# Performance work log

Measured on AMD Instinct MI355X. Metric: run time of the kernel, lower is better.

The kernel has to match this reference:

```python
import jax, jax.numpy as jnp
import numpy as np

B, C, L = 4, 64, 4096
RED = 4          # reduction -> q/k channels = C // RED = 16
N_HASHES = 4
HASH_BUCKETS = min(L // 4, 32)  # = 32, matches torch code
EPS = 1e-5


def _conv1x1(x, W, b):
    # x: [B, Cin, L], W: [Cout, Cin], b: [Cout]
    return jnp.einsum('bcl,oc->bol', x, W) + b[None, :, None]


def setup_inputs() -> dict:
    key = jax.random.key(0)
    ks = jax.random.split(key, 12)
    Cq = C // RED
    x = jax.random.normal(ks[0], (B, C, L), dtype=jnp.float32)
    hash_idx = jax.random.randint(ks[1], (B, N_HASHES, L), 0, HASH_BUCKETS, dtype=jnp.int32)
    sC = 1.0 / np.sqrt(C)
    Wq = jax.random.normal(ks[2], (Cq, C), dtype=jnp.float32) * sC
    bq = jax.random.normal(ks[3], (Cq,), dtype=jnp.float32) * 0.01
    Wk = jax.random.normal(ks[4], (Cq, C), dtype=jnp.float32) * sC
    bk = jax.random.normal(ks[5], (Cq,), dtype=jnp.float32) * 0.01
    Wv = jax.random.normal(ks[6], (C, C), dtype=jnp.float32) * sC
    bv = jax.random.normal(ks[7], (C,), dtype=jnp.float32) * 0.01
    Wo = jax.random.normal(ks[8], (C, C), dtype=jnp.float32) * sC
    bo = jax.random.normal(ks[9], (C,), dtype=jnp.float32) * 0.01
    gamma = jax.random.normal(ks[10], (1,), dtype=jnp.float32)  # nonzero so attn path matters
    bn_w = jnp.ones((C,), dtype=jnp.float32)
    bn_b = jnp.zeros((C,), dtype=jnp.float32)
    return dict(x=x, hash_idx=hash_idx, Wq=Wq, bq=bq, Wk=Wk, bk=bk,
                Wv=Wv, bv=bv, Wo=Wo, bo=bo, gamma=gamma, bn_w=bn_w, bn_b=bn_b)


def reference(x, hash_idx, Wq, bq, Wk, bk, Wv, bv, Wo, bo, gamma, bn_w, bn_b):
    # 1x1 conv projections
    q = _conv1x1(x, Wq, bq)   # [B, C/RED, L]
    k = _conv1x1(x, Wk, bk)   # [B, C/RED, L]
    v = _conv1x1(x, Wv, bv)   # [B, C, L]

    qT = q.transpose(0, 2, 1)  # [B, L, Cq]
    kT = k.transpose(0, 2, 1)
    vT = v.transpose(0, 2, 1)  # [B, L, C]

    # raw scores are hash-independent; only the bucket mask changes per hash
    scores = jnp.einsum('bic,bjc->bij', qT, kT)  # [B, L, L], no sqrt(d) scaling (matches torch)

    n_hashes = hash_idx.shape[1]
    acc = jnp.zeros_like(vT)
    for h in range(n_hashes):  # small fixed loop
        idx = hash_idx[:, h, :]                       # [B, L]
        mask = idx[:, :, None] == idx[:, None, :]     # same-bucket mask [B, L, L]
        s = jnp.where(mask, scores, -1e9)
        attn = jax.nn.softmax(s, axis=-1)             # within-bucket softmax (diag always valid)
        acc = acc + jnp.einsum('bij,bjc->bic', attn, vT)
    attn_out = (acc / n_hashes).transpose(0, 2, 1)    # [B, C, L], averaged over hashes

    out = _conv1x1(attn_out, Wo, bo)
    out = gamma * out + x                             # residual with learned scalar

    # BatchNorm1d, training mode: biased batch stats over (B, L) per channel
    mean = out.mean(axis=(0, 2), keepdims=True)
    var = out.var(axis=(0, 2), keepdims=True)
    out = (out - mean) * jax.lax.rsqrt(var + EPS)
    out = out * bn_w[None, :, None] + bn_b[None, :, None]
    return out
```

## Files before the change

### kernel.cpp

```cpp
#include <hip/hip_runtime.h>
#include <math.h>

#define Bn 4
#define Cn 64
#define Ln 4096
#define CQ 16
#define NH 4
#define NB 32
#define EPSV 1e-5f

#define MAXS 384
#define CH2 64
#define KSTR 20
#define VSTR 64

#define QSPLIT 2
#define QSTRIDE (64*QSPLIT)

#define QSZ   (Bn*Ln*CQ)
#define VSZ   (Bn*Ln*Cn)
#define ACCSZ (Bn*Ln*Cn)
#define NBH   (Bn*NH)

#define OFF_K   QSZ
#define OFF_V   (2*QSZ)
#define OFF_ACC (2*QSZ + VSZ)

#define LOG2E 1.44269504088896f

__global__ __launch_bounds__(256) void proj_kernel(
        const float* __restrict__ x,
        const float* __restrict__ Wq, const float* __restrict__ bq,
        const float* __restrict__ Wk, const float* __restrict__ bk,
        const float* __restrict__ Wv, const float* __restrict__ bv,
        float* __restrict__ q, float* __restrict__ k, float* __restrict__ v) {
    __shared__ float sWt[Cn*32];
    __shared__ float sb[32];
    int tid = threadIdx.x;
    int third = blockIdx.x % 3;
    int pg    = blockIdx.x / 3;
    int rbase = third * 32;
    for (int idx = tid; idx < Cn*32; idx += 256) {
        int rr = idx & 31, c = idx >> 5;
        int r = rbase + rr;
        float w;
        if (r < 16)      w = Wq[r*Cn + c];
        else if (r < 32) w = Wk[(r-16)*Cn + c];
        else             w = Wv[(r-32)*Cn + c];
        sWt[c*32 + rr] = w;
    }
    if (tid < 32) {
        int r = rbase + tid;
        sb[tid] = (r < 16) ? bq[r] : (r < 32 ? bk[r-16] : bv[r-32]);
    }
    __syncthreads();
    int p = tid & 63, og = tid >> 6;
    int gp = pg * 64 + p;
    int b = gp >> 12, l = gp & (Ln - 1);
    const float* xp = &x[b*Cn*Ln + l];
    int rr0 = og * 8;
    float val[8];
    #pragma unroll
    for (int i = 0; i < 8; i++) val[i] = sb[rr0 + i];
    #pragma unroll
    for (int c0 = 0; c0 < Cn; c0 += 8) {
        float xv[8];
        #pragma unroll
        for (int i = 0; i < 8; i++) xv[i] = xp[(c0 + i)*Ln];
        #pragma unroll
        for (int i = 0; i < 8; i++) {
            const float* wrow = &sWt[(c0 + i)*32 + rr0];
            #pragma unroll
            for (int j = 0; j < 8; j++) val[j] = fmaf(wrow[j], xv[i], val[j]);
        }
    }
    int f = third*8 + og*2;
    float4 t0 = make_float4(val[0], val[1], val[2], val[3]);
    float4 t1 = make_float4(val[4], val[5], val[6], val[7]);
    float4* q4 = (float4*)&q[gp*CQ];
    float4* k4 = (float4*)&k[gp*CQ];
    float4* v4 = (float4*)&v[gp*Cn];
    if (f < 4)      { q4[f]   = t0; q4[f+1] = t1; }
    else if (f < 8) { k4[f-4] = t0; k4[f-3] = t1; }
    else            { v4[f-8] = t0; v4[f-7] = t1; }
}

__device__ __forceinline__ float quad_reduce_sum(float d) {
    d += __int_as_float(__builtin_amdgcn_mov_dpp(__float_as_int(d), 0xB1, 0xF, 0xF, true));
    d += __int_as_float(__builtin_amdgcn_mov_dpp(__float_as_int(d), 0x4E, 0xF, 0xF, true));
    return d;
}

template<int NS, int MODE>
__device__ __forceinline__ void attn_pass(
        int qbase, int S, int b, int h, int tid, int rem,
        const int* list, float* ks, float* vs,
        const float* __restrict__ q, const float* __restrict__ k,
        const float* __restrict__ v, float* __restrict__ acc) {
    int qd = tid >> 2, c4 = tid & 3;
    float4 qr[NS];
    float4 o[NS][4];
    float lsum[NS];
    int qi[NS], iqr[NS];
    #pragma unroll
    for (int s = 0; s < NS; s++) {
        qi[s] = qbase + QSTRIDE*s + qd;
        iqr[s] = 0;
        lsum[s] = 0.f;
        #pragma unroll
        for (int i = 0; i < 4; i++) o[s][i] = make_float4(0.f,0.f,0.f,0.f);
        if (qi[s] < S) {
            iqr[s] = list[qi[s]];
            const float4* qp = (const float4*)&q[((size_t)b*Ln + iqr[s])*CQ];
            float4 t = qp[c4];
            t.x*=LOG2E; t.y*=LOG2E; t.z*=LOG2E; t.w*=LOG2E;
            qr[s] = t;
        } else {
            qr[s] = make_float4(0.f,0.f,0.f,0.f);
        }
    }
    for (int cc = 0; cc < S; cc += CH2) {
        int nk = min(CH2, S - cc);
        __syncthreads();
        {
            int jj = tid >> 2, cf = tid & 3;
            if (jj < nk) {
                const float4* kp = (const float4*)&k[((size_t)b*Ln + list[cc+jj])*CQ];
                *(float4*)&ks[jj*KSTR + cf*4] = kp[cf];
            }
        }
        #pragma unroll
        for (int uu = 0; uu < 4; uu++) {
            int idx = uu*256 + tid;
            int jj = idx >> 4, cf = idx & 15;
            if (jj < nk) {
                const float4* vp = (const float4*)&v[((size_t)b*Ln + list[cc+jj])*Cn];
                *(float4*)&vs[jj*VSTR + cf*4] = vp[cf];
            }
        }
        __syncthreads();
        if (rem > 0) {
            for (int j = 0; j < nk; j++) {
                float4 kq = *(const float4*)&ks[j*KSTR + c4*4];
                const float4* vp4 = (const float4*)&vs[j*VSTR + c4*16];
                float4 v0 = vp4[0], v1 = vp4[1], v2 = vp4[2], v3 = vp4[3];
                #pragma unroll
                for (int s = 0; s < NS; s++) {
                    float d = qr[s].x*kq.x;
                    d = fmaf(qr[s].y, kq.y, d);
                    d = fmaf(qr[s].z, kq.z, d);
                    d = fmaf(qr[s].w, kq.w, d);
                    d = quad_reduce_sum(d);
                    float pw = __builtin_amdgcn_exp2f(d);
                    lsum[s] += pw;
                    o[s][0].x = fmaf(pw, v0.x, o[s][0].x); o[s][0].y = fmaf(pw, v0.y, o[s][0].y);
                    o[s][0].z = fmaf(pw, v0.z, o[s][0].z); o[s][0].w = fmaf(pw, v0.w, o[s][0].w);
                    o[s][1].x = fmaf(pw, v1.x, o[s][1].x); o[s][1].y = fmaf(pw, v1.y, o[s][1].y);
                    o[s][1].z = fmaf(pw, v1.z, o[s][1].z); o[s][1].w = fmaf(pw, v1.w, o[s][1].w);
                    o[s][2].x = fmaf(pw, v2.x, o[s][2].x); o[s][2].y = fmaf(pw, v2.y, o[s][2].y);
                    o[s][2].z = fmaf(pw, v2.z, o[s][2].z); o[s][2].w = fmaf(pw, v2.w, o[s][2].w);
                    o[s][3].x = fmaf(pw, v3.x, o[s][3].x); o[s][3].y = fmaf(pw, v3.y, o[s][3].y);
                    o[s][3].z = fmaf(pw, v3.z, o[s][3].z); o[s][3].w = fmaf(pw, v3.w, o[s][3].w);
                }
            }
        }
    }
    #pragma unroll
    for (int s = 0; s < NS; s++) {
        if (qi[s] < S) {
            float inv = 1.f / lsum[s];
            #pragma unroll
            for (int i = 0; i < 4; i++) {
                o[s][i].x*=inv; o[s][i].y*=inv; o[s][i].z*=inv; o[s][i].w*=inv;
            }
            if (MODE == 1) {
                float4* ap = (float4*)&acc[((size_t)h*Bn*Ln + b*Ln + iqr[s])*Cn + c4*16];
                ap[0]=o[s][0]; ap[1]=o[s][1]; ap[2]=o[s][2]; ap[3]=o[s][3];
            } else {
                float* ap = &acc[((size_t)b*Ln + iqr[s])*Cn + c4*16];
                #pragma unroll
                for (int i = 0; i < 4; i++) {
                    atomicAdd(&ap[4*i+0], (&o[s][i].x)[0]);
                    atomicAdd(&ap[4*i+1], (&o[s][i].x)[1]);
                    atomicAdd(&ap[4*i+2], (&o[s][i].x)[2]);
                    atomicAdd(&ap[4*i+3], (&o[s][i].x)[3]);
                }
            }
        }
    }
}

template<int MODE>
__global__ __launch_bounds__(256, 4) void attn_kernel(
        const float* __restrict__ q, const float* __restrict__ k,
        const float* __restrict__ v, const int* __restrict__ hidx,
        float* __restrict__ acc) {
    __shared__ int list[MAXS];
    __shared__ float ks[CH2*KSTR];
    __shared__ float vs[CH2*VSTR];
    __shared__ int wtot[4];
    int blk = blockIdx.x;
    int qs = blk >> 9;
    int u  = blk & (NB-1);
    int bh = (blk >> 5) & (NBH-1);
    int b  = bh >> 2;
    int h  = bh & 3;
    int tid = threadIdx.x;

    const int4* hp4 = (const int4*)(&hidx[bh*Ln] + tid*16);
    int hv[16];
    #pragma unroll
    for (int t = 0; t < 4; t++) {
        int4 tmp = hp4[t];
        hv[t*4+0]=tmp.x; hv[t*4+1]=tmp.y; hv[t*4+2]=tmp.z; hv[t*4+3]=tmp.w;
    }
    int myCnt = 0;
    #pragma unroll
    for (int t = 0; t < 16; t++) myCnt += (hv[t] == u);
    int lane = tid & 63, wv = tid >> 6;
    int pre = myCnt;
    #pragma unroll
    for (int d = 1; d < 64; d <<= 1) {
        int t = __shfl_up(pre, d, 64);
        if (lane >= d) pre += t;
    }
    if (lane == 63) wtot[wv] = pre;
    __syncthreads();
    int base = 0;
    #pragma unroll
    for (int w = 0; w < 4; w++) base += (w < wv) ? wtot[w] : 0;
    int Sall = wtot[0] + wtot[1] + wtot[2] + wtot[3];
    int S = min(Sall, MAXS);
    int excl = base + pre - myCnt;
    #pragma unroll
    for (int t = 0; t < 16; t++) {
        if (hv[t] == u) {
            if (excl < MAXS) list[excl] = tid*16 + t;
            excl++;
        }
    }
    __syncthreads();

    int wq0 = (tid >> 6) << 4;
    for (int qbase = qs*64; qbase < S; qbase += 3*QSTRIDE) {
        int rem = S - qbase - wq0;
        if (rem > 2*QSTRIDE)      attn_pass<3,MODE>(qbase,S,b,h,tid,rem,list,ks,vs,q,k,v,acc);
        else if (rem > QSTRIDE)   attn_pass<2,MODE>(qbase,S,b,h,tid,rem,list,ks,vs,q,k,v,acc);
        else                      attn_pass<1,MODE>(qbase,S,b,h,tid,rem,list,ks,vs,q,k,v,acc);
    }
}

template<int MODE>
__global__ __launch_bounds__(256) void outconv_kernel(
        const float* __restrict__ acc, const float* __restrict__ Wo,
        const float* __restrict__ bo, const float* __restrict__ gamma,
        const float* __restrict__ x, float* __restrict__ y) {
    __shared__ float sWt[Cn*Cn];
    __shared__ float sA[Cn*33];
    __shared__ float sb[Cn];
    int tid = threadIdx.x;
    int pg = blockIdx.x;
    for (int idx = tid; idx < Cn*Cn; idx += 256) {
        int o = idx & 63, c = idx >> 6;
        sWt[c*Cn + o] = Wo[o*Cn + c];
    }
    if (tid < Cn) sb[tid] = bo[tid];
    const float4* a4 = (const float4*)&acc[(size_t)pg*32*Cn];
    #pragma unroll
    for (int r = 0; r < 2; r++) {
        int idx = r*256 + tid;
        int p = idx >> 4, c0 = (idx & 15) * 4;
        float4 t = a4[idx];
        if (MODE == 1) {
            float4 t1 = a4[(size_t)ACCSZ/4   + idx];
            float4 t2 = a4[(size_t)ACCSZ/4*2 + idx];
            float4 t3 = a4[(size_t)ACCSZ/4*3 + idx];
            t.x += t1.x + t2.x + t3.x; t.y += t1.y + t2.y + t3.y;
            t.z += t1.z + t2.z + t3.z; t.w += t1.w + t2.w + t3.w;
        }
        sA[(c0+0)*33 + p] = t.x*0.25f;
        sA[(c0+1)*33 + p] = t.y*0.25f;
        sA[(c0+2)*33 + p] = t.z*0.25f;
        sA[(c0+3)*33 + p] = t.w*0.25f;
    }
    __syncthreads();
    float g = gamma[0];
    int p = tid & 31, og = tid >> 5;
    int gp = pg * 32 + p;
    int b = gp >> 12, l = gp & (Ln - 1);
    int o0 = og * 8;
    float val[8];
    #pragma unroll
    for (int i = 0; i < 8; i++) val[i] = sb[o0 + i];
    #pragma unroll
    for (int c = 0; c < Cn; c++) {
        float av = sA[c*33 + p];
        const float* wrow = &sWt[c*Cn + o0];
        #pragma unroll
        for (int i = 0; i < 8; i++) val[i] = fmaf(wrow[i], av, val[i]);
    }
    #pragma unroll
    for (int i = 0; i < 8; i++) {
        int o = o0 + i;
        float yv = fmaf(g, val[i], x[(b*Cn + o)*Ln + l]);
        y[(b*Cn + o)*Ln + l] = yv;
    }
}

__global__ __launch_bounds__(256) void stats_kernel(
        const float* __restrict__ y, float* __restrict__ ssumP, float* __restrict__ ssqP) {
    int c = blockIdx.x >> 2;
    int part = blockIdx.x & 3;
    int tid = threadIdx.x;
    const float4* yp = (const float4*)&y[(part*Cn + c)*Ln];
    float s = 0.f, s2 = 0.f;
    #pragma unroll
    for (int i = 0; i < 4; i++) {
        float4 t = yp[i*256 + tid];
        s  += t.x + t.y + t.z + t.w;
        s2 += t.x*t.x + t.y*t.y + t.z*t.z + t.w*t.w;
    }
    #pragma unroll
    for (int w = 1; w < 64; w <<= 1) {
        s  += __shfl_xor(s,  w, 64);
        s2 += __shfl_xor(s2, w, 64);
    }
    __shared__ float rs[4], rs2[4];
    int wv = tid >> 6;
    if ((tid & 63) == 0) { rs[wv] = s; rs2[wv] = s2; }
    __syncthreads();
    if (tid == 0) {
        ssumP[blockIdx.x] = rs[0]+rs[1]+rs[2]+rs[3];
        ssqP[blockIdx.x]  = rs2[0]+rs2[1]+rs2[2]+rs2[3];
    }
}

__global__ __launch_bounds__(256) void norm_kernel(
        const float* __restrict__ y,
        const float* __restrict__ ssumP, const float* __restrict__ ssqP,
        const float* __restrict__ bnw, const float* __restrict__ bnb,
        float* __restrict__ out) {
    int idx = blockIdx.x * 256 + threadIdx.x;
    int flat = idx * 4;
    int c = (flat / Ln) & 63;
    float s = 0.f, s2 = 0.f;
    #pragma unroll
    for (int hh = 0; hh < 4; hh++) { s += ssumP[c*4+hh]; s2 += ssqP[c*4+hh]; }
    const float n = (float)(Bn*Ln);
    float mu = s / n;
    float var = s2 / n - mu*mu;
    float is = rsqrtf(var + EPSV);
    float w = is * bnw[c];
    float bb = bnb[c] - mu * w;
    float4 t = ((const float4*)y)[idx];
    float4 r;
    r.x = t.x*w + bb; r.y = t.y*w + bb; r.z = t.z*w + bb; r.w = t.w*w + bb;
    ((float4*)out)[idx] = r;
}

extern "C" void kernel_launch(void* const* d_in, const int* in_sizes, int n_in,
                              void* d_out, int out_size, void* d_ws, size_t ws_size,
                              hipStream_t stream) {
    const float* x    = (const float*)d_in[0];
    const int*   hidx = (const int*)  d_in[1];
    const float* Wq   = (const float*)d_in[2];
    const float* bq   = (const float*)d_in[3];
    const float* Wk   = (const float*)d_in[4];
    const float* bk   = (const float*)d_in[5];
    const float* Wv   = (const float*)d_in[6];
    const float* bv   = (const float*)d_in[7];
    const float* Wo   = (const float*)d_in[8];
    const float* bo   = (const float*)d_in[9];
    const float* gam  = (const float*)d_in[10];
    const float* bnw  = (const float*)d_in[11];
    const float* bnb  = (const float*)d_in[12];
    float* out = (float*)d_out;

    float* ws  = (float*)d_ws;
    float* q   = ws;
    float* k   = ws + OFF_K;
    float* v   = ws + OFF_V;
    float* acc = ws + OFF_ACC;
    float* y   = ws;

    const size_t bigNeed = ((size_t)OFF_ACC + 4*(size_t)ACCSZ + 512) * sizeof(float);
    bool big = ws_size >= bigNeed;
    float* ssumP = acc + (big ? 4*(size_t)ACCSZ : (size_t)ACCSZ);
    float* ssqP  = ssumP + 256;

    proj_kernel<<<Bn*Ln/64*3, 256, 0, stream>>>(x, Wq, bq, Wk, bk, Wv, bv, q, k, v);
    if (big) {
        attn_kernel<1><<<NBH*NB*QSPLIT, 256, 0, stream>>>(q, k, v, hidx, acc);
        outconv_kernel<1><<<Bn*Ln/32, 256, 0, stream>>>(acc, Wo, bo, gam, x, y);
    } else {
        hipMemsetAsync(acc, 0, (size_t)ACCSZ*sizeof(float), stream);
        attn_kernel<0><<<NBH*NB*QSPLIT, 256, 0, stream>>>(q, k, v, hidx, acc);
        outconv_kernel<0><<<Bn*Ln/32, 256, 0, stream>>>(acc, Wo, bo, gam, x, y);
    }
    stats_kernel<<<Cn*4, 256, 0, stream>>>(y, ssumP, ssqP);
    norm_kernel<<<Bn*Cn*Ln/4/256, 256, 0, stream>>>(y, ssumP, ssqP, bnw, bnb, out);
}
```

Baseline: 155.2 us.

## Restructure bucket attention to stage whole bucket KV once and split keys across lanes

The attention kernel now launches one block per (batch, hash, bucket) instead of two query-split blocks. It stages the whole bucket's K and V into shared memory in one pass when the bucket fits in 192 entries, and falls back to chunked staging otherwise. Inside a wave, lanes are split across four queries and four key sub-streams; partial sums are combined with DPP row reductions at the end, and only one lane group writes results. This is meant to cut repeated KV staging and per-chunk barriers, at the cost of half as many blocks, a lower occupancy hint, extra reduction shuffles and masked tail handling. Separately, the weight rows in the projection and output-conv kernels are now read from shared memory as float4 loads.

```diff
diff --git a/kernel.cpp b/kernel.cpp
--- a/kernel.cpp
+++ b/kernel.cpp
@@ -10,12 +10,7 @@
 #define EPSV 1e-5f
 
 #define MAXS 384
-#define CH2 64
-#define KSTR 20
-#define VSTR 64
-
-#define QSPLIT 2
-#define QSTRIDE (64*QSPLIT)
+#define SFULL 192
 
 #define QSZ   (Bn*Ln*CQ)
 #define VSZ   (Bn*Ln*Cn)
@@ -69,9 +64,13 @@
         for (int i = 0; i < 8; i++) xv[i] = xp[(c0 + i)*Ln];
         #pragma unroll
         for (int i = 0; i < 8; i++) {
-            const float* wrow = &sWt[(c0 + i)*32 + rr0];
-            #pragma unroll
-            for (int j = 0; j < 8; j++) val[j] = fmaf(wrow[j], xv[i], val[j]);
+            const float4 wa = *(const float4*)&sWt[(c0 + i)*32 + rr0];
+            const float4 wb = *(const float4*)&sWt[(c0 + i)*32 + rr0 + 4];
+            float xvi = xv[i];
+            val[0] = fmaf(wa.x, xvi, val[0]); val[1] = fmaf(wa.y, xvi, val[1]);
+            val[2] = fmaf(wa.z, xvi, val[2]); val[3] = fmaf(wa.w, xvi, val[3]);
+            val[4] = fmaf(wb.x, xvi, val[4]); val[5] = fmaf(wb.y, xvi, val[5]);
+            val[6] = fmaf(wb.z, xvi, val[6]); val[7] = fmaf(wb.w, xvi, val[7]);
         }
     }
     int f = third*8 + og*2;
@@ -91,118 +90,145 @@
     return d;
 }
 
-template<int NS, int MODE>
-__device__ __forceinline__ void attn_pass(
-        int qbase, int S, int b, int h, int tid, int rem,
-        const int* list, float* ks, float* vs,
-        const float* __restrict__ q, const float* __restrict__ k,
-        const float* __restrict__ v, float* __restrict__ acc) {
-    int qd = tid >> 2, c4 = tid & 3;
-    float4 qr[NS];
-    float4 o[NS][4];
-    float lsum[NS];
-    int qi[NS], iqr[NS];
-    #pragma unroll
-    for (int s = 0; s < NS; s++) {
-        qi[s] = qbase + QSTRIDE*s + qd;
-        iqr[s] = 0;
-        lsum[s] = 0.f;
+__device__ __forceinline__ float rowsum16(float x) {
+    x += __int_as_float(__builtin_amdgcn_mov_dpp(__float_as_int(x), 0x114, 0xF, 0xF, true));
+    x += __int_as_float(__builtin_amdgcn_mov_dpp(__float_as_int(x), 0x118, 0xF, 0xF, true));
+    return x;
+}
+
+struct SweepState {
+    float4 qr[4];
+    float4 o[4][4];
+    float  lsum[4];
+    int    ir[4];
+    int    qact[4];
+};
+
+__device__ __forceinline__ void sweep_init(SweepState& st, int q0, int S, int act,
+        const int* list, const float4* Q4, int qq, int c4) {
+    #pragma unroll
+    for (int s = 0; s < 4; s++) {
+        int qi = q0 + s*4 + qq;
+        int a = act && (qi < S);
+        st.qact[s] = a;
+        int r = a ? list[qi] : 0;
+        st.ir[s] = r;
+        float4 t = make_float4(0.f, 0.f, 0.f, 0.f);
+        if (a) {
+            t = Q4[(size_t)r*4 + c4];
+            t.x *= LOG2E; t.y *= LOG2E; t.z *= LOG2E; t.w *= LOG2E;
+        }
+        st.qr[s] = t;
+        st.lsum[s] = 0.f;
         #pragma unroll
-        for (int i = 0; i < 4; i++) o[s][i] = make_float4(0.f,0.f,0.f,0.f);
-        if (qi[s] < S) {
-            iqr[s] = list[qi[s]];
-            const float4* qp = (const float4*)&q[((size_t)b*Ln + iqr[s])*CQ];
-            float4 t = qp[c4];
-            t.x*=LOG2E; t.y*=LOG2E; t.z*=LOG2E; t.w*=LOG2E;
-            qr[s] = t;
-        } else {
-            qr[s] = make_float4(0.f,0.f,0.f,0.f);
-        }
-    }
-    for (int cc = 0; cc < S; cc += CH2) {
-        int nk = min(CH2, S - cc);
-        __syncthreads();
-        {
-            int jj = tid >> 2, cf = tid & 3;
-            if (jj < nk) {
-                const float4* kp = (const float4*)&k[((size_t)b*Ln + list[cc+jj])*CQ];
-                *(float4*)&ks[jj*KSTR + cf*4] = kp[cf];
-            }
-        }
+        for (int tt = 0; tt < 4; tt++) st.o[s][tt] = make_float4(0.f, 0.f, 0.f, 0.f);
+    }
+}
+
+template<bool MASKED>
+__device__ __forceinline__ void kb_step(SweepState& st, int kb, int nkv,
+        const float4* ks4, const float4* vs4, int l15, int kk,
+        int i0, int i1, int i2, int i3) {
+    const float4 kq = ks4[kb*16 + l15];
+    const float4 va = vs4[kb*64 + i0*16 + l15];
+    const float4 vb = vs4[kb*64 + i1*16 + l15];
+    const float4 vc = vs4[kb*64 + i2*16 + l15];
+    const float4 vd = vs4[kb*64 + i3*16 + l15];
+    #pragma unroll
+    for (int s = 0; s < 4; s++) {
+        float d = st.qr[s].x * kq.x;
+        d = fmaf(st.qr[s].y, kq.y, d);
+        d = fmaf(st.qr[s].z, kq.z, d);
+        d = fmaf(st.qr[s].w, kq.w, d);
+        d = quad_reduce_sum(d);
+        float pw = __builtin_amdgcn_exp2f(d);
+        if (MASKED) pw = ((kb*4 + kk) < nkv) ? pw : 0.f;
+        st.lsum[s] += pw;
+        st.o[s][0].x = fmaf(pw, va.x, st.o[s][0].x); st.o[s][0].y = fmaf(pw, va.y, st.o[s][0].y);
+        st.o[s][0].z = fmaf(pw, va.z, st.o[s][0].z); st.o[s][0].w = fmaf(pw, va.w, st.o[s][0].w);
+        st.o[s][1].x = fmaf(pw, vb.x, st.o[s][1].x); st.o[s][1].y = fmaf(pw, vb.y, st.o[s][1].y);
+        st.o[s][1].z = fmaf(pw, vb.z, st.o[s][1].z); st.o[s][1].w = fmaf(pw, vb.w, st.o[s][1].w);
+        st.o[s][2].x = fmaf(pw, vc.x, st.o[s][2].x); st.o[s][2].y = fmaf(pw, vc.y, st.o[s][2].y);
+        st.o[s][2].z = fmaf(pw, vc.z, st.o[s][2].z); st.o[s][2].w = fmaf(pw, vc.w, st.o[s][2].w);
+        st.o[s][3].x = fmaf(pw, vd.x, st.o[s][3].x); st.o[s][3].y = fmaf(pw, vd.y, st.o[s][3].y);
+        st.o[s][3].z = fmaf(pw, vd.z, st.o[s][3].z); st.o[s][3].w = fmaf(pw, vd.w, st.o[s][3].w);
+    }
+}
+
+__device__ __forceinline__ void sweep_keys(SweepState& st, int nk,
+        const float4* ks4, const float4* vs4, int l15, int kk,
+        int i0, int i1, int i2, int i3) {
+    int nf = nk >> 2;
+    for (int kb = 0; kb < nf; kb++)
+        kb_step<false>(st, kb, nk, ks4, vs4, l15, kk, i0, i1, i2, i3);
+    if (nk & 3)
+        kb_step<true>(st, nf, nk, ks4, vs4, l15, kk, i0, i1, i2, i3);
+}
+
+template<int MODE>
+__device__ __forceinline__ void sweep_fin(SweepState& st, float* __restrict__ acc,
+        int b, int h, int qq, int lane, int c4) {
+    #pragma unroll
+    for (int s = 0; s < 4; s++) {
+        st.lsum[s] = rowsum16(st.lsum[s]);
         #pragma unroll
-        for (int uu = 0; uu < 4; uu++) {
-            int idx = uu*256 + tid;
-            int jj = idx >> 4, cf = idx & 15;
-            if (jj < nk) {
-                const float4* vp = (const float4*)&v[((size_t)b*Ln + list[cc+jj])*Cn];
-                *(float4*)&vs[jj*VSTR + cf*4] = vp[cf];
-            }
-        }
-        __syncthreads();
-        if (rem > 0) {
-            for (int j = 0; j < nk; j++) {
-                float4 kq = *(const float4*)&ks[j*KSTR + c4*4];
-                const float4* vp4 = (const float4*)&vs[j*VSTR + c4*16];
-                float4 v0 = vp4[0], v1 = vp4[1], v2 = vp4[2], v3 = vp4[3];
-                #pragma unroll
-                for (int s = 0; s < NS; s++) {
-                    float d = qr[s].x*kq.x;
-                    d = fmaf(qr[s].y, kq.y, d);
-                    d = fmaf(qr[s].z, kq.z, d);
-                    d = fmaf(qr[s].w, kq.w, d);
-                    d = quad_reduce_sum(d);
-                    float pw = __builtin_amdgcn_exp2f(d);
-                    lsum[s] += pw;
-                    o[s][0].x = fmaf(pw, v0.x, o[s][0].x); o[s][0].y = fmaf(pw, v0.y, o[s][0].y);
-                    o[s][0].z = fmaf(pw, v0.z, o[s][0].z); o[s][0].w = fmaf(pw, v0.w, o[s][0].w);
-                    o[s][1].x = fmaf(pw, v1.x, o[s][1].x); o[s][1].y = fmaf(pw, v1.y, o[s][1].y);
-                    o[s][1].z = fmaf(pw, v1.z, o[s][1].z); o[s][1].w = fmaf(pw, v1.w, o[s][1].w);
-                    o[s][2].x = fmaf(pw, v2.x, o[s][2].x); o[s][2].y = fmaf(pw, v2.y, o[s][2].y);
-                    o[s][2].z = fmaf(pw, v2.z, o[s][2].z); o[s][2].w = fmaf(pw, v2.w, o[s][2].w);
-                    o[s][3].x = fmaf(pw, v3.x, o[s][3].x); o[s][3].y = fmaf(pw, v3.y, o[s][3].y);
-                    o[s][3].z = fmaf(pw, v3.z, o[s][3].z); o[s][3].w = fmaf(pw, v3.w, o[s][3].w);
+        for (int t = 0; t < 4; t++) {
+            st.o[s][t].x = rowsum16(st.o[s][t].x);
+            st.o[s][t].y = rowsum16(st.o[s][t].y);
+            st.o[s][t].z = rowsum16(st.o[s][t].z);
+            st.o[s][t].w = rowsum16(st.o[s][t].w);
+        }
+    }
+    if ((lane & 15) < 12) return;
+    #pragma unroll
+    for (int s = 0; s < 4; s++) {
+        if (st.qact[s]) {
+            float inv = 1.f / st.lsum[s];
+            #pragma unroll
+            for (int t = 0; t < 4; t++) {
+                float4 r;
+                r.x = st.o[s][t].x * inv; r.y = st.o[s][t].y * inv;
+                r.z = st.o[s][t].z * inv; r.w = st.o[s][t].w * inv;
+                int ch = ((qq + t) & 3)*16 + c4*4;
+                if (MODE == 1) {
+                    *(float4*)&acc[(((size_t)h*Bn + b)*Ln + st.ir[s])*Cn + ch] = r;
+                } else {
+                    float* ap = &acc[((size_t)b*Ln + st.ir[s])*Cn + ch];
+                    atomicAdd(&ap[0], r.x); atomicAdd(&ap[1], r.y);
+                    atomicAdd(&ap[2], r.z); atomicAdd(&ap[3], r.w);
                 }
             }
         }
     }
-    #pragma unroll
-    for (int s = 0; s < NS; s++) {
-        if (qi[s] < S) {
-            float inv = 1.f / lsum[s];
-            #pragma unroll
-            for (int i = 0; i < 4; i++) {
-                o[s][i].x*=inv; o[s][i].y*=inv; o[s][i].z*=inv; o[s][i].w*=inv;
-            }
-            if (MODE == 1) {
-                float4* ap = (float4*)&acc[((size_t)h*Bn*Ln + b*Ln + iqr[s])*Cn + c4*16];
-                ap[0]=o[s][0]; ap[1]=o[s][1]; ap[2]=o[s][2]; ap[3]=o[s][3];
-            } else {
-                float* ap = &acc[((size_t)b*Ln + iqr[s])*Cn + c4*16];
-                #pragma unroll
-                for (int i = 0; i < 4; i++) {
-                    atomicAdd(&ap[4*i+0], (&o[s][i].x)[0]);
-                    atomicAdd(&ap[4*i+1], (&o[s][i].x)[1]);
-                    atomicAdd(&ap[4*i+2], (&o[s][i].x)[2]);
-                    atomicAdd(&ap[4*i+3], (&o[s][i].x)[3]);
-                }
-            }
-        }
+}
+
+__device__ __forceinline__ void stage_kv(int tid, int nk, int k0, const int* list,
+        const float4* K4, const float4* V4, float4* ks4, float4* vs4) {
+    const float4 z = make_float4(0.f, 0.f, 0.f, 0.f);
+    int nb4 = (nk + 3) >> 2;
+    for (int G = tid; G < nb4*16; G += 256) {
+        int j = G >> 2;
+        ks4[G] = (j < nk) ? K4[(size_t)list[k0 + j]*4 + (G & 3)] : z;
+    }
+    for (int F = tid; F < nb4*64; F += 256) {
+        int kb = F >> 6, ii = (F >> 4) & 3, k2 = (F >> 2) & 3, cc = F & 3;
+        int j = kb*4 + k2;
+        vs4[F] = (j < nk) ? V4[(size_t)list[k0 + j]*16 + ii*4 + cc] : z;
     }
 }
 
 template<int MODE>
-__global__ __launch_bounds__(256, 4) void attn_kernel(
+__global__ __launch_bounds__(256, 2) void attn_kernel(
         const float* __restrict__ q, const float* __restrict__ k,
         const float* __restrict__ v, const int* __restrict__ hidx,
         float* __restrict__ acc) {
     __shared__ int list[MAXS];
-    __shared__ float ks[CH2*KSTR];
-    __shared__ float vs[CH2*VSTR];
     __shared__ int wtot[4];
+    __shared__ float4 ks4[SFULL*4];
+    __shared__ float4 vs4[SFULL*16];
     int blk = blockIdx.x;
-    int qs = blk >> 9;
     int u  = blk & (NB-1);
-    int bh = (blk >> 5) & (NBH-1);
+    int bh = blk >> 5;
     int b  = bh >> 2;
     int h  = bh & 3;
     int tid = threadIdx.x;
@@ -241,12 +267,39 @@
     }
     __syncthreads();
 
-    int wq0 = (tid >> 6) << 4;
-    for (int qbase = qs*64; qbase < S; qbase += 3*QSTRIDE) {
-        int rem = S - qbase - wq0;
-        if (rem > 2*QSTRIDE)      attn_pass<3,MODE>(qbase,S,b,h,tid,rem,list,ks,vs,q,k,v,acc);
-        else if (rem > QSTRIDE)   attn_pass<2,MODE>(qbase,S,b,h,tid,rem,list,ks,vs,q,k,v,acc);
-        else                      attn_pass<1,MODE>(qbase,S,b,h,tid,rem,list,ks,vs,q,k,v,acc);
+    int qq = (lane >> 4) & 3;
+    int kk = (lane >> 2) & 3;
+    int c4 = lane & 3;
+    int l15 = lane & 15;
+    int i0 = qq, i1 = (qq+1)&3, i2 = (qq+2)&3, i3 = (qq+3)&3;
+    const float4* Q4 = (const float4*)&q[(size_t)b*Ln*CQ];
+    const float4* K4 = (const float4*)&k[(size_t)b*Ln*CQ];
+    const float4* V4 = (const float4*)&v[(size_t)b*Ln*Cn];
+
+    if (S <= SFULL) {
+        stage_kv(tid, S, 0, list, K4, V4, ks4, vs4);
+        __syncthreads();
+        for (int q0 = wv*16; q0 < S; q0 += 64) {
+            SweepState st;
+            sweep_init(st, q0, S, 1, list, Q4, qq, c4);
+            sweep_keys(st, S, ks4, vs4, l15, kk, i0, i1, i2, i3);
+            sweep_fin<MODE>(st, acc, b, h, qq, lane, c4);
+        }
+    } else {
+        for (int q0s = 0; q0s < S; q0s += 64) {
+            int q0 = q0s + wv*16;
+            int act = q0 < S;
+            SweepState st;
+            sweep_init(st, q0, S, act, list, Q4, qq, c4);
+            for (int k0 = 0; k0 < S; k0 += SFULL) {
+                int nk = min(SFULL, S - k0);
+                __syncthreads();
+                stage_kv(tid, nk, k0, list, K4, V4, ks4, vs4);
+                __syncthreads();
+                if (act) sweep_keys(st, nk, ks4, vs4, l15, kk, i0, i1, i2, i3);
+            }
+            if (act) sweep_fin<MODE>(st, acc, b, h, qq, lane, c4);
+        }
     }
 }
 
@@ -295,9 +348,12 @@
     #pragma unroll
     for (int c = 0; c < Cn; c++) {
         float av = sA[c*33 + p];
-        const float* wrow = &sWt[c*Cn + o0];
-        #pragma unroll
-        for (int i = 0; i < 8; i++) val[i] = fmaf(wrow[i], av, val[i]);
+        const float4 wa = *(const float4*)&sWt[c*Cn + o0];
+        const float4 wb = *(const float4*)&sWt[c*Cn + o0 + 4];
+        val[0] = fmaf(wa.x, av, val[0]); val[1] = fmaf(wa.y, av, val[1]);
+        val[2] = fmaf(wa.z, av, val[2]); val[3] = fmaf(wa.w, av, val[3]);
+        val[4] = fmaf(wb.x, av, val[4]); val[5] = fmaf(wb.y, av, val[5]);
+        val[6] = fmaf(wb.z, av, val[6]); val[7] = fmaf(wb.w, av, val[7]);
     }
     #pragma unroll
     for (int i = 0; i < 8; i++) {
@@ -390,11 +446,11 @@
 
     proj_kernel<<<Bn*Ln/64*3, 256, 0, stream>>>(x, Wq, bq, Wk, bk, Wv, bv, q, k, v);
     if (big) {
-        attn_kernel<1><<<NBH*NB*QSPLIT, 256, 0, stream>>>(q, k, v, hidx, acc);
+        attn_kernel<1><<<NBH*NB, 256, 0, stream>>>(q, k, v, hidx, acc);
         outconv_kernel<1><<<Bn*Ln/32, 256, 0, stream>>>(acc, Wo, bo, gam, x, y);
     } else {
         hipMemsetAsync(acc, 0, (size_t)ACCSZ*sizeof(float), stream);
-        attn_kernel<0><<<NBH*NB*QSPLIT, 256, 0, stream>>>(q, k, v, hidx, acc);
+        attn_kernel<0><<<NBH*NB, 256, 0, stream>>>(q, k, v, hidx, acc);
         outconv_kernel<0><<<Bn*Ln/32, 256, 0, stream>>>(acc, Wo, bo, gam, x, y);
     }
     stats_kernel<<<Cn*4, 256, 0, stream>>>(y, ssumP, ssqP);
```

Measured after the change: 157.5 us. Within noise of the previous version (+1.5%).
